# Kernel tuning notes

Hardware: AMD Instinct MI355X
Metric: run time of the kernel (lower is better)

Reference implementation:

```python
import jax, jax.numpy as jnp
import numpy as np
from jax import lax

V, E, H, L = 32000, 512, 512, 2
B, S, T = 64, 128, 64


def setup_inputs() -> dict:
    key = jax.random.key(0)
    ks = jax.random.split(key, 16)
    sc = 0.05  # weight scale to keep gates/tanh in a sane range
    inp = {
        "tokens": jax.random.randint(ks[0], (T, B), 0, V, dtype=jnp.int32),
        "memory_bank": jax.random.normal(ks[1], (B, S, H), dtype=jnp.float32),
        "lengths": jax.random.randint(ks[2], (B,), 1, S + 1, dtype=jnp.int32),
        "h0": jax.random.normal(ks[3], (L, B, H), dtype=jnp.float32),
        "c0": jax.random.normal(ks[4], (L, B, H), dtype=jnp.float32),
        "embedding": jax.random.normal(ks[5], (V, E), dtype=jnp.float32),
        "w_ih0": jax.random.normal(ks[6], (4 * H, E + H), dtype=jnp.float32) * sc,
        "w_hh0": jax.random.normal(ks[7], (4 * H, H), dtype=jnp.float32) * sc,
        "b_ih0": jax.random.normal(ks[8], (4 * H,), dtype=jnp.float32) * sc,
        "b_hh0": jax.random.normal(ks[9], (4 * H,), dtype=jnp.float32) * sc,
        "w_ih1": jax.random.normal(ks[10], (4 * H, H), dtype=jnp.float32) * sc,
        "w_hh1": jax.random.normal(ks[11], (4 * H, H), dtype=jnp.float32) * sc,
        "b_ih1": jax.random.normal(ks[12], (4 * H,), dtype=jnp.float32) * sc,
        "b_hh1": jax.random.normal(ks[13], (4 * H,), dtype=jnp.float32) * sc,
        "w_in": jax.random.normal(ks[14], (H, H), dtype=jnp.float32) * sc,
        "w_out": jax.random.normal(ks[15], (H, 2 * H), dtype=jnp.float32) * sc,
    }
    return inp


def _lstm_cell(x, h, c, w_ih, w_hh, b_ih, b_hh):
    # PyTorch LSTMCell: gates in (i, f, g, o) order
    g = x @ w_ih.T + b_ih + h @ w_hh.T + b_hh
    i, f, gg, o = jnp.split(g, 4, axis=-1)
    c_new = jax.nn.sigmoid(f) * c + jax.nn.sigmoid(i) * jnp.tanh(gg)
    h_new = jax.nn.sigmoid(o) * jnp.tanh(c_new)
    return h_new, c_new


def reference(tokens, memory_bank, lengths, h0, c0, embedding,
              w_ih0, w_hh0, b_ih0, b_hh0, w_ih1, w_hh1, b_ih1, b_hh1,
              w_in, w_out):
    Bn, Sn, Hn = memory_bank.shape
    mask = jnp.arange(Sn)[None, :] < lengths[:, None]  # [B, S]

    def step(carry, tok):
        h, c, feed = carry  # h, c: [L, B, H]; feed: [B, H]
        emb = jnp.take(embedding, tok, axis=0)           # [B, E]
        x = jnp.concatenate([emb, feed], axis=-1)        # [B, E+H]
        h0n, c0n = _lstm_cell(x, h[0], c[0], w_ih0, w_hh0, b_ih0, b_hh0)
        h1n, c1n = _lstm_cell(h0n, h[1], c[1], w_ih1, w_hh1, b_ih1, b_hh1)
        rnn_out = h1n                                    # [B, H]
        # Luong general attention
        q = rnn_out @ w_in.T                             # [B, H]
        scores = jnp.einsum('bh,bsh->bs', q, memory_bank)
        scores = jnp.where(mask, scores, -jnp.inf)
        p = jax.nn.softmax(scores, axis=-1)              # [B, S]
        ctx = jnp.einsum('bs,bsh->bh', p, memory_bank)   # [B, H]
        attn_h = jnp.tanh(jnp.concatenate([ctx, rnn_out], axis=-1) @ w_out.T)
        new_carry = (jnp.stack([h0n, h1n]), jnp.stack([c0n, c1n]), attn_h)
        return new_carry, (attn_h, p)

    feed0 = jnp.zeros((Bn, Hn), dtype=memory_bank.dtype)
    (h_f, c_f, _), (dec_outs, attns) = lax.scan(step, (h0, c0, feed0), tokens)
    return dec_outs, attns, h_f, c_f
```

## Files before the change

kernel.cpp:

```cpp
#include <hip/hip_runtime.h>
#include <hip/hip_bf16.h>

typedef __bf16 bf16x8 __attribute__((ext_vector_type(8)));
typedef unsigned short u16x8 __attribute__((ext_vector_type(8)));
typedef float f32x4 __attribute__((ext_vector_type(4)));

constexpr int TT = 64;
constexpr int BB = 64;
constexpr int SS = 128;
constexpr int HH = 512;
constexpr int GG = 2048;

constexpr int NW0E = 2048 * 512;
constexpr int NW0R = 2048 * 1024;
constexpr int NW1  = 2048 * 512;
constexpr int NWO  = 512 * 1024;
constexpr int NWI  = 512 * 512;

struct P {
  const int* tok; const float* mbank; const int* len;
  const float* h0_in; const float* c0_in; const float* emb;
  const float* w_ih0; const float* w_hh0; const float* b_ih0; const float* b_hh0;
  const float* w_ih1; const float* w_hh1; const float* b_ih1; const float* b_hh1;
  const float* w_in; const float* w_out;
  float* out_dec; float* out_attn; float* out_hf; float* out_cf;
  unsigned short *W0E, *W0R, *Wih1, *Whh1, *Wout, *WinT;
  float *EGb;
  float *Mw;
  float *b0, *b1, *h0buf, *h1s, *c0s, *c1s, *feed, *part1, *ctx, *scg;
  unsigned int* flag;
};

__device__ __forceinline__ unsigned short f2bf(float f) {
  unsigned int u = __builtin_bit_cast(unsigned int, f);
  return (unsigned short)((u + 0x7fffu + ((u >> 16) & 1u)) >> 16);
}
__device__ __forceinline__ float bf2f(unsigned short h) {
  return __builtin_bit_cast(float, ((unsigned int)h) << 16);
}
__device__ __forceinline__ bf16x8 ldb(const unsigned short* p) {
  return __builtin_bit_cast(bf16x8, *(const u16x8*)p);
}
__device__ __forceinline__ f32x4 mfma_(bf16x8 a, bf16x8 b, f32x4 c) {
  return __builtin_amdgcn_mfma_f32_16x16x32_bf16(a, b, c, 0, 0, 0);
}
__device__ __forceinline__ float sigm(float x) { return 1.f / (1.f + __expf(-x)); }
__device__ __forceinline__ f32x4 zero4() { f32x4 z = {0.f, 0.f, 0.f, 0.f}; return z; }

#define ATL(pp) __hip_atomic_load((pp), __ATOMIC_RELAXED, __HIP_MEMORY_SCOPE_AGENT)
#define ATS(pp, vv) __hip_atomic_store((pp), (vv), __ATOMIC_RELAXED, __HIP_MEMORY_SCOPE_AGENT)
#define ATA(pp, vv) __hip_atomic_fetch_add((pp), (vv), __ATOMIC_RELAXED, __HIP_MEMORY_SCOPE_AGENT)

__device__ __forceinline__ void splitA(const float* s, bf16x8& hi, bf16x8& lo) {
  float4 a0 = *(const float4*)s;
  float4 a1 = *(const float4*)(s + 4);
  float v[8] = {a0.x, a0.y, a0.z, a0.w, a1.x, a1.y, a1.z, a1.w};
  u16x8 h, l;
#pragma unroll
  for (int j = 0; j < 8; ++j) {
    unsigned short hb = f2bf(v[j]);
    h[j] = hb;
    l[j] = f2bf(v[j] - bf2f(hb));
  }
  hi = __builtin_bit_cast(bf16x8, h);
  lo = __builtin_bit_cast(bf16x8, l);
}
__device__ __forceinline__ f32x4 mfma3(bf16x8 ah, bf16x8 al, bf16x8 bh, bf16x8 bl, f32x4 c) {
  c = mfma_(al, bh, c);
  c = mfma_(ah, bl, c);
  c = mfma_(ah, bh, c);
  return c;
}

__global__ void prep_weights(P p) {
  constexpr int TOT = NW0E + NW0R + NW1 + NW1 + NWO + NWI + 2048 + 2048 +
                      32768 * 5 + 8192 + 1024;
  for (int i = blockIdx.x * blockDim.x + threadIdx.x; i < TOT;
       i += gridDim.x * blockDim.x) {
    int j = i;
    float v; unsigned short* dst; int N;
    if (j < NW0E) {
      int n = j >> 9, k = j & 511;
      v = p.w_ih0[n * 1024 + k];
      dst = p.W0E; N = NW0E; goto split;
    }
    j -= NW0E;
    if (j < NW0R) {
      int n = j >> 10, k = j & 1023;
      v = (k < 512) ? p.w_ih0[n * 1024 + 512 + k] : p.w_hh0[n * 512 + (k - 512)];
      dst = p.W0R; N = NW0R; goto split;
    }
    j -= NW0R;
    if (j < NW1) { v = p.w_ih1[j]; dst = p.Wih1; N = NW1; goto split; }
    j -= NW1;
    if (j < NW1) { v = p.w_hh1[j]; dst = p.Whh1; N = NW1; goto split; }
    j -= NW1;
    if (j < NWO) { v = p.w_out[j]; dst = p.Wout; N = NWO; goto split; }
    j -= NWO;
    if (j < NWI) {
      int n = j >> 9, q = j & 511;
      v = p.w_in[q * 512 + n];
      dst = p.WinT; N = NWI; goto split;
    }
    j -= NWI;
    if (j < 2048) { p.b0[j] = p.b_ih0[j] + p.b_hh0[j]; continue; }
    j -= 2048;
    if (j < 2048) { p.b1[j] = p.b_ih1[j] + p.b_hh1[j]; continue; }
    j -= 2048;
    if (j < 32768) { p.h0buf[j] = p.h0_in[j]; continue; }
    j -= 32768;
    if (j < 32768) { p.h1s[j] = p.h0_in[32768 + j]; continue; }
    j -= 32768;
    if (j < 32768) { p.c0s[j] = p.c0_in[j]; continue; }
    j -= 32768;
    if (j < 32768) { p.c1s[j] = p.c0_in[32768 + j]; continue; }
    j -= 32768;
    if (j < 32768) { p.feed[j] = 0.f; continue; }
    j -= 32768;
    if (j < 8192) { p.scg[j] = 0.f; continue; }
    j -= 8192;
    p.flag[j] = 0u;
    continue;
  split:
    {
      unsigned short hb = f2bf(v);
      dst[j] = hb;
      dst[N + j] = f2bf(v - bf2f(hb));
    }
  }
}

__global__ void prep_mw(P p) {
  const int wg = blockIdx.x;
  const int bm = wg & 127, bn = wg >> 7;
  const int tid = threadIdx.x, wave = tid >> 6, lane = tid & 63;
  const int arow = lane & 15, kq = (lane >> 4) * 8;
  const int m0 = bm * 64 + wave * 16;
  const int n0 = bn * 16;
  const float* A = p.mbank + (size_t)(m0 + arow) * HH;
  const unsigned short* Bp = p.WinT + (size_t)(n0 + arow) * HH + kq;
  f32x4 acc = zero4();
  for (int kk = 0; kk < HH; kk += 32) {
    bf16x8 ah, al;
    splitA(A + kk + kq, ah, al);
    acc = mfma3(ah, al, ldb(Bp + kk), ldb(Bp + NWI + kk), acc);
  }
  const int r0 = m0 + (lane >> 4) * 4;
#pragma unroll
  for (int r = 0; r < 4; ++r)
    p.Mw[(size_t)(r0 + r) * HH + n0 + arow] = acc[r];
}

__global__ void prep_eg(P p) {
  const int wg = blockIdx.x;
  const int bn = wg & 127, bm = wg >> 7;
  const int tid = threadIdx.x, wave = tid >> 6, lane = tid & 63;
  const int arow = lane & 15, kq = (lane >> 4) * 8;
  const int m0 = bm * 64 + wave * 16;
  const int n0 = bn * 16;
  const int token = p.tok[m0 + arow];
  const float* A = p.emb + (size_t)token * 512;
  const unsigned short* Bp = p.W0E + (size_t)(n0 + arow) * 512 + kq;
  f32x4 acc = zero4();
  for (int kk = 0; kk < 512; kk += 32) {
    bf16x8 ah, al;
    splitA(A + kk + kq, ah, al);
    acc = mfma3(ah, al, ldb(Bp + kk), ldb(Bp + NW0E + kk), acc);
  }
  const int r0 = m0 + (lane >> 4) * 4;
  const float bb = p.b0[n0 + arow];
#pragma unroll
  for (int r = 0; r < 4; ++r)
    p.EGb[(size_t)(r0 + r) * 2048 + n0 + arow] = acc[r] + bb;
}

__global__ void __launch_bounds__(256) decoder_main(P p) {
  const int wg = blockIdx.x, tid = threadIdx.x;
  const int wave = tid >> 6, lane = tid & 63;
  const int arow = lane & 15;
  const int kq = (lane >> 4) * 8;
  const int g = wg >> 6;
  const int u = wg & 63;
  unsigned nb = 0;

  __shared__ unsigned short MbHi[32][512];
  __shared__ unsigned short MbLo[32][512];
  __shared__ float Aslab[16][516];
  __shared__ float exch[4][16][16];
  __shared__ float scl[128];
  __shared__ float pl[128];

  const int attb = (g << 4) + (u >> 2);
  const int attq = u & 3;

  for (int idx = tid; idx < 32 * 512; idx += 256) {
    int r = idx >> 9, c = idx & 511;
    float v = p.mbank[(size_t)(attb * 128 + attq * 32 + r) * 512 + c];
    unsigned short hb = f2bf(v);
    MbHi[r][c] = hb;
    MbLo[r][c] = f2bf(v - bf2f(hb));
  }
  float mwreg[8][8];
  {
    const float* mwb = p.Mw + (size_t)(attb * 128 + attq * 32 + wave * 8) * 512 + lane * 8;
#pragma unroll
    for (int i = 0; i < 8; ++i) {
      float4 a = *(const float4*)(mwb + i * 512);
      float4 b = *(const float4*)(mwb + i * 512 + 4);
      mwreg[i][0] = a.x; mwreg[i][1] = a.y; mwreg[i][2] = a.z; mwreg[i][3] = a.w;
      mwreg[i][4] = b.x; mwreg[i][5] = b.y; mwreg[i][6] = b.z; mwreg[i][7] = b.w;
    }
  }

  const int w2 = (u < 32) ? u : u - 32;
  const int strip = w2;
  const int gate = wave;
  const int colj = strip * 16 + arow;
  const int rowbase = g * 16 * 512;

  unsigned* slots = p.flag + 128 + g * 128;
  auto gbar = [&]() {
    ++nb;
    asm volatile("s_waitcnt vmcnt(0)" ::: "memory");
    __syncthreads();
    if (tid == 0) ATS(&slots[u], nb);
    for (;;) {
      unsigned v = (tid < 64) ? ATL(&slots[tid]) : nb;
      if (__syncthreads_count((int)(v < nb)) == 0) break;
    }
  };

  auto stageC = [&](const float* base) {
    __syncthreads();
    float4 v[8];
    const float* ap[8];
#pragma unroll
    for (int j = 0; j < 8; ++j) {
      int idx = tid * 4 + j * 1024;
      ap[j] = base + (idx >> 9) * 512 + (idx & 511);
    }
#pragma unroll
    for (int j = 0; j < 8; ++j)
      asm volatile("global_load_dwordx4 %0, %1, off sc1" : "=v"(v[j]) : "v"(ap[j]));
    asm volatile("s_waitcnt vmcnt(0)" ::: "memory");
    __builtin_amdgcn_sched_barrier(0);
#pragma unroll
    for (int j = 0; j < 8; ++j) {
      int idx = tid * 4 + j * 1024;
      *(float4*)&Aslab[idx >> 9][idx & 511] = v[j];
    }
    __syncthreads();
  };
  auto gemm_half = [&](const unsigned short* whi, const unsigned short* wlo,
                       f32x4 acc) {
#pragma unroll 4
    for (int kk = 0; kk < 512; kk += 32) {
      bf16x8 ah, al;
      splitA(&Aslab[arow][kk + kq], ah, al);
      acc = mfma3(ah, al, ldb(whi + kk), ldb(wlo + kk), acc);
    }
    return acc;
  };

  for (int t = 0; t < TT; ++t) {
    const float* h0c = p.h0buf + (t & 1) * (BB * HH);
    float* h0n = p.h0buf + ((t + 1) & 1) * (BB * HH);

    if (u < 32) {
      const size_t wr = (size_t)(gate * 512 + colj) * 1024;
      f32x4 acc = zero4();
      stageC(p.feed + rowbase);
      acc = gemm_half(p.W0R + wr + kq, p.W0R + NW0R + wr + kq, acc);
      stageC(h0c + rowbase);
      acc = gemm_half(p.W0R + wr + 512 + kq, p.W0R + NW0R + wr + 512 + kq, acc);
      const float* eg =
          p.EGb + ((size_t)(t * 64 + g * 16)) * 2048 + gate * 512 + colj;
#pragma unroll
      for (int r = 0; r < 4; ++r) {
        acc[r] += eg[((lane >> 4) * 4 + r) * 2048];
        exch[gate][(lane >> 4) * 4 + r][arow] = acc[r];
      }
      __syncthreads();
      {
        int br = tid >> 4, nc = tid & 15;
        int idx = rowbase + br * 512 + strip * 16 + nc;
        float iv = sigm(exch[0][br][nc]);
        float fv = sigm(exch[1][br][nc]);
        float gv = tanhf(exch[2][br][nc]);
        float ov = sigm(exch[3][br][nc]);
        float cn = fv * p.c0s[idx] + iv * gv;
        p.c0s[idx] = cn;
        float hv = ov * tanhf(cn);
        ATS(&h0n[idx], hv);
        if (t == TT - 1) { p.out_cf[idx] = cn; p.out_hf[idx] = hv; }
      }
    } else {
      const size_t wr = (size_t)(gate * 512 + colj) * 512;
      stageC(p.h1s + rowbase);
      f32x4 acc = gemm_half(p.Whh1 + wr + kq, p.Whh1 + NW1 + wr + kq, zero4());
      const float bb = p.b1[gate * 512 + colj];
#pragma unroll
      for (int r = 0; r < 4; ++r)
        ATS(&p.part1[(g * 16 + (lane >> 4) * 4 + r) * 2048 + gate * 512 + colj],
            acc[r] + bb);
    }
    gbar();

    if (u < 32) {
      const size_t wr = (size_t)(gate * 512 + colj) * 512;
      stageC(h0n + rowbase);
      f32x4 acc = gemm_half(p.Wih1 + wr + kq, p.Wih1 + NW1 + wr + kq, zero4());
#pragma unroll
      for (int r = 0; r < 4; ++r) {
        acc[r] += ATL(&p.part1[(g * 16 + (lane >> 4) * 4 + r) * 2048 +
                               gate * 512 + colj]);
        exch[gate][(lane >> 4) * 4 + r][arow] = acc[r];
      }
      __syncthreads();
      {
        int br = tid >> 4, nc = tid & 15;
        int idx = rowbase + br * 512 + strip * 16 + nc;
        float iv = sigm(exch[0][br][nc]);
        float fv = sigm(exch[1][br][nc]);
        float gv = tanhf(exch[2][br][nc]);
        float ov = sigm(exch[3][br][nc]);
        float cn = fv * p.c1s[idx] + iv * gv;
        p.c1s[idx] = cn;
        float hv = ov * tanhf(cn);
        ATS(&p.h1s[idx], hv);
        if (t == TT - 1) { p.out_cf[BB * HH + idx] = cn; p.out_hf[BB * HH + idx] = hv; }
      }
    } else {
      int base = g * 8192 + (u - 32) * 256 + tid;
      ATS(&p.ctx[base], 0.f);
    }
    gbar();

    {
      float h8[8];
      {
        const float* hp = p.h1s + attb * 512 + lane * 8;
        float4 a, c;
        asm volatile("global_load_dwordx4 %0, %1, off sc1" : "=v"(a) : "v"(hp));
        asm volatile("global_load_dwordx4 %0, %1, off sc1" : "=v"(c) : "v"(hp + 4));
        asm volatile("s_waitcnt vmcnt(0)" ::: "memory");
        __builtin_amdgcn_sched_barrier(0);
        h8[0] = a.x; h8[1] = a.y; h8[2] = a.z; h8[3] = a.w;
        h8[4] = c.x; h8[5] = c.y; h8[6] = c.z; h8[7] = c.w;
      }
#pragma unroll
      for (int i = 0; i < 8; ++i) {
        const int sl = wave * 8 + i;
        float d = h8[0] * mwreg[i][0] + h8[1] * mwreg[i][1] +
                  h8[2] * mwreg[i][2] + h8[3] * mwreg[i][3] +
                  h8[4] * mwreg[i][4] + h8[5] * mwreg[i][5] +
                  h8[6] * mwreg[i][6] + h8[7] * mwreg[i][7];
#pragma unroll
        for (int o = 32; o; o >>= 1) d += __shfl_xor(d, o);
        if (lane == 0) ATS(&p.scg[attb * 128 + attq * 32 + sl], d);
      }
      asm volatile("s_waitcnt vmcnt(0)" ::: "memory");
      __syncthreads();
      if (tid == 0) {
        ATA(&p.flag[attb], 1u);
        const unsigned tgt = 4u * (unsigned)(t + 1);
        while (ATL(&p.flag[attb]) < tgt) __builtin_amdgcn_s_sleep(1);
      }
      __syncthreads();
      if (tid < 128) scl[tid] = ATL(&p.scg[attb * 128 + tid]);
      __syncthreads();
      if (wave == 0) {
        const int lenb = p.len[attb];
        float s0 = (lane < lenb) ? scl[lane] : -__builtin_inff();
        float s1 = (lane + 64 < lenb) ? scl[lane + 64] : -__builtin_inff();
        float mx = fmaxf(s0, s1);
#pragma unroll
        for (int o = 32; o; o >>= 1) mx = fmaxf(mx, __shfl_xor(mx, o));
        float e0 = (lane < lenb) ? __expf(s0 - mx) : 0.f;
        float e1 = (lane + 64 < lenb) ? __expf(s1 - mx) : 0.f;
        float sm = e0 + e1;
#pragma unroll
        for (int o = 32; o; o >>= 1) sm += __shfl_xor(sm, o);
        float inv = 1.f / sm;
        pl[lane] = e0 * inv; pl[lane + 64] = e1 * inv;
        if (attq == 0) {
          float* ao = p.out_attn + ((size_t)t * BB + attb) * SS;
          ao[lane] = e0 * inv; ao[lane + 64] = e1 * inv;
        }
      }
      __syncthreads();
      {
        const int h2 = tid * 2;
        float ca = 0.f, cb = 0.f;
#pragma unroll 4
        for (int s = 0; s < 32; ++s) {
          float ps = pl[attq * 32 + s];
          unsigned vh = *(const unsigned*)&MbHi[s][h2];
          unsigned vl = *(const unsigned*)&MbLo[s][h2];
          ca += ps * (bf2f((unsigned short)(vh & 0xffffu)) +
                      bf2f((unsigned short)(vl & 0xffffu)));
          cb += ps * (bf2f((unsigned short)(vh >> 16)) +
                      bf2f((unsigned short)(vl >> 16)));
        }
        atomicAdd(&p.ctx[attb * 512 + h2], ca);
        atomicAdd(&p.ctx[attb * 512 + h2 + 1], cb);
      }
    }
    gbar();

    if (u < 8) {
      const int nstrip = u * 4 + wave;
      const int cj = nstrip * 16 + arow;
      const size_t wr = (size_t)cj * 1024;
      f32x4 acc = zero4();
      stageC(p.ctx + rowbase);
      acc = gemm_half(p.Wout + wr + kq, p.Wout + NWO + wr + kq, acc);
      stageC(p.h1s + rowbase);
      acc = gemm_half(p.Wout + wr + 512 + kq, p.Wout + NWO + wr + 512 + kq, acc);
      float* dec = p.out_dec + (size_t)t * BB * HH;
#pragma unroll
      for (int r = 0; r < 4; ++r) {
        int b = g * 16 + (lane >> 4) * 4 + r;
        float v = tanhf(acc[r]);
        dec[b * 512 + cj] = v;
        ATS(&p.feed[b * 512 + cj], v);
      }
    }
    gbar();
  }
}

extern "C" void kernel_launch(void* const* d_in, const int* in_sizes, int n_in,
                              void* d_out, int out_size, void* d_ws, size_t ws_size,
                              hipStream_t stream) {
  P p;
  p.tok   = (const int*)d_in[0];
  p.mbank = (const float*)d_in[1];
  p.len   = (const int*)d_in[2];
  p.h0_in = (const float*)d_in[3];
  p.c0_in = (const float*)d_in[4];
  p.emb   = (const float*)d_in[5];
  p.w_ih0 = (const float*)d_in[6];
  p.w_hh0 = (const float*)d_in[7];
  p.b_ih0 = (const float*)d_in[8];
  p.b_hh0 = (const float*)d_in[9];
  p.w_ih1 = (const float*)d_in[10];
  p.w_hh1 = (const float*)d_in[11];
  p.b_ih1 = (const float*)d_in[12];
  p.b_hh1 = (const float*)d_in[13];
  p.w_in  = (const float*)d_in[14];
  p.w_out = (const float*)d_in[15];

  float* out = (float*)d_out;
  p.out_dec  = out;
  p.out_attn = out + (size_t)TT * BB * HH;
  p.out_hf   = out + (size_t)TT * BB * HH + (size_t)TT * BB * SS;
  p.out_cf   = p.out_hf + 2 * BB * HH;

  char* w = (char*)d_ws;
  auto alloc = [&](size_t n) { char* r = w; w += (n + 255) & ~(size_t)255; return r; };
  p.W0E   = (unsigned short*)alloc((size_t)NW0E * 2 * 2);
  p.W0R   = (unsigned short*)alloc((size_t)NW0R * 2 * 2);
  p.Wih1  = (unsigned short*)alloc((size_t)NW1 * 2 * 2);
  p.Whh1  = (unsigned short*)alloc((size_t)NW1 * 2 * 2);
  p.Wout  = (unsigned short*)alloc((size_t)NWO * 2 * 2);
  p.WinT  = (unsigned short*)alloc((size_t)NWI * 2 * 2);
  p.EGb   = (float*)alloc((size_t)4096 * 2048 * 4);
  p.Mw    = (float*)alloc((size_t)BB * SS * HH * 4);
  p.b0    = (float*)alloc(2048 * 4);
  p.b1    = (float*)alloc(2048 * 4);
  p.h0buf = (float*)alloc((size_t)2 * BB * HH * 4);
  p.h1s   = (float*)alloc((size_t)BB * HH * 4);
  p.c0s   = (float*)alloc((size_t)BB * HH * 4);
  p.c1s   = (float*)alloc((size_t)BB * HH * 4);
  p.feed  = (float*)alloc((size_t)BB * HH * 4);
  p.part1 = (float*)alloc((size_t)BB * GG * 4);
  p.ctx   = (float*)alloc((size_t)BB * HH * 4);
  p.scg   = (float*)alloc((size_t)BB * SS * 4);
  p.flag  = (unsigned int*)alloc(1024 * 4);

  hipLaunchKernelGGL(prep_weights, dim3(4096), dim3(256), 0, stream, p);
  hipLaunchKernelGGL(prep_mw, dim3(4096), dim3(256), 0, stream, p);
  hipLaunchKernelGGL(prep_eg, dim3(8192), dim3(256), 0, stream, p);

  void* args[] = {(void*)&p};
  hipError_t ce = hipLaunchCooperativeKernel((void*)decoder_main, dim3(256),
                                             dim3(256), args, 0, stream);
  if (ce != hipSuccess) {
    (void)hipGetLastError();
    hipLaunchKernelGGL(decoder_main, dim3(256), dim3(256), 0, stream, p);
  }
}
```

Measured before the change: 3.525 ms.

## Fuse output projection into attention blocks with per-batch flag sync

```diff
diff --git a/kernel.cpp b/kernel.cpp
--- a/kernel.cpp
+++ b/kernel.cpp
@@ -24,7 +24,8 @@
   const float* w_ih1; const float* w_hh1; const float* b_ih1; const float* b_hh1;
   const float* w_in; const float* w_out;
   float* out_dec; float* out_attn; float* out_hf; float* out_cf;
-  unsigned short *W0E, *W0R, *Wih1, *Whh1, *Wout, *WinT;
+  unsigned short *W0E, *W0R, *Wih1, *Whh1, *WinT;
+  float *WoutT;
   float *EGb;
   float *Mw;
   float *b0, *b1, *h0buf, *h1s, *c0s, *c1s, *feed, *part1, *ctx, *scg;
@@ -95,7 +96,11 @@
     j -= NW1;
     if (j < NW1) { v = p.w_hh1[j]; dst = p.Whh1; N = NW1; goto split; }
     j -= NW1;
-    if (j < NWO) { v = p.w_out[j]; dst = p.Wout; N = NWO; goto split; }
+    if (j < NWO) {
+      int k = j >> 9, n = j & 511;
+      p.WoutT[j] = p.w_out[n * 1024 + k];
+      continue;
+    }
     j -= NWO;
     if (j < NWI) {
       int n = j >> 9, q = j & 511;
@@ -189,6 +194,7 @@
   __shared__ float exch[4][16][16];
   __shared__ float scl[128];
   __shared__ float pl[128];
+  __shared__ float prj[1024];
 
   const int attb = (g << 4) + (u >> 2);
   const int attq = u & 3;
@@ -229,6 +235,15 @@
       if (__syncthreads_count((int)(v < nb)) == 0) break;
     }
   };
+  auto fsync = [&](unsigned* f, unsigned tgt) {
+    asm volatile("s_waitcnt vmcnt(0)" ::: "memory");
+    __syncthreads();
+    if (tid == 0) {
+      ATA(f, 1u);
+      while (ATL(f) < tgt) __builtin_amdgcn_s_sleep(1);
+    }
+    __syncthreads();
+  };
 
   auto stageC = [&](const float* base) {
     __syncthreads();
@@ -268,16 +283,19 @@
 
     if (u < 32) {
       const size_t wr = (size_t)(gate * 512 + colj) * 1024;
+      const float* eg =
+          p.EGb + ((size_t)(t * 64 + g * 16)) * 2048 + gate * 512 + colj;
+      float egv[4];
+#pragma unroll
+      for (int r = 0; r < 4; ++r) egv[r] = eg[((lane >> 4) * 4 + r) * 2048];
       f32x4 acc = zero4();
       stageC(p.feed + rowbase);
       acc = gemm_half(p.W0R + wr + kq, p.W0R + NW0R + wr + kq, acc);
       stageC(h0c + rowbase);
       acc = gemm_half(p.W0R + wr + 512 + kq, p.W0R + NW0R + wr + 512 + kq, acc);
-      const float* eg =
-          p.EGb + ((size_t)(t * 64 + g * 16)) * 2048 + gate * 512 + colj;
 #pragma unroll
       for (int r = 0; r < 4; ++r) {
-        acc[r] += eg[((lane >> 4) * 4 + r) * 2048];
+        acc[r] += egv[r];
         exch[gate][(lane >> 4) * 4 + r][arow] = acc[r];
       }
       __syncthreads();
@@ -308,12 +326,16 @@
 
     if (u < 32) {
       const size_t wr = (size_t)(gate * 512 + colj) * 512;
+      float pv[4];
+#pragma unroll
+      for (int r = 0; r < 4; ++r)
+        pv[r] = ATL(&p.part1[(g * 16 + (lane >> 4) * 4 + r) * 2048 +
+                             gate * 512 + colj]);
       stageC(h0n + rowbase);
       f32x4 acc = gemm_half(p.Wih1 + wr + kq, p.Wih1 + NW1 + wr + kq, zero4());
 #pragma unroll
       for (int r = 0; r < 4; ++r) {
-        acc[r] += ATL(&p.part1[(g * 16 + (lane >> 4) * 4 + r) * 2048 +
-                               gate * 512 + colj]);
+        acc[r] += pv[r];
         exch[gate][(lane >> 4) * 4 + r][arow] = acc[r];
       }
       __syncthreads();
@@ -359,14 +381,7 @@
         for (int o = 32; o; o >>= 1) d += __shfl_xor(d, o);
         if (lane == 0) ATS(&p.scg[attb * 128 + attq * 32 + sl], d);
       }
-      asm volatile("s_waitcnt vmcnt(0)" ::: "memory");
-      __syncthreads();
-      if (tid == 0) {
-        ATA(&p.flag[attb], 1u);
-        const unsigned tgt = 4u * (unsigned)(t + 1);
-        while (ATL(&p.flag[attb]) < tgt) __builtin_amdgcn_s_sleep(1);
-      }
-      __syncthreads();
+      fsync(&p.flag[attb], 4u * (unsigned)(t + 1));
       if (tid < 128) scl[tid] = ATL(&p.scg[attb * 128 + tid]);
       __syncthreads();
       if (wave == 0) {
@@ -387,6 +402,8 @@
           float* ao = p.out_attn + ((size_t)t * BB + attb) * SS;
           ao[lane] = e0 * inv; ao[lane + 64] = e1 * inv;
         }
+        *(float4*)&prj[512 + lane * 8]     = make_float4(h8[0], h8[1], h8[2], h8[3]);
+        *(float4*)&prj[512 + lane * 8 + 4] = make_float4(h8[4], h8[5], h8[6], h8[7]);
       }
       __syncthreads();
       {
@@ -405,25 +422,29 @@
         atomicAdd(&p.ctx[attb * 512 + h2], ca);
         atomicAdd(&p.ctx[attb * 512 + h2 + 1], cb);
       }
-    }
-    gbar();
-
-    if (u < 8) {
-      const int nstrip = u * 4 + wave;
-      const int cj = nstrip * 16 + arow;
-      const size_t wr = (size_t)cj * 1024;
-      f32x4 acc = zero4();
-      stageC(p.ctx + rowbase);
-      acc = gemm_half(p.Wout + wr + kq, p.Wout + NWO + wr + kq, acc);
-      stageC(p.h1s + rowbase);
-      acc = gemm_half(p.Wout + wr + 512 + kq, p.Wout + NWO + wr + 512 + kq, acc);
-      float* dec = p.out_dec + (size_t)t * BB * HH;
-#pragma unroll
-      for (int r = 0; r < 4; ++r) {
-        int b = g * 16 + (lane >> 4) * 4 + r;
-        float v = tanhf(acc[r]);
-        dec[b * 512 + cj] = v;
-        ATS(&p.feed[b * 512 + cj], v);
+      fsync(&p.flag[64 + attb], 4u * (unsigned)(t + 1));
+      {
+        prj[tid * 2]     = ATL(&p.ctx[attb * 512 + tid * 2]);
+        prj[tid * 2 + 1] = ATL(&p.ctx[attb * 512 + tid * 2 + 1]);
+      }
+      __syncthreads();
+      {
+        const int jc = attq * 128 + (tid & 127);
+        const int kh = tid >> 7;
+        const float* wt = p.WoutT + jc;
+        float d = 0.f;
+#pragma unroll 8
+        for (int k = kh * 512; k < kh * 512 + 512; ++k)
+          d = fmaf(prj[k], wt[(size_t)k * 512], d);
+        float* exf = (float*)exch;
+        if (kh == 1) exf[tid - 128] = d;
+        __syncthreads();
+        if (kh == 0) {
+          d += exf[tid];
+          float v = tanhf(d);
+          p.out_dec[(size_t)t * BB * HH + attb * 512 + jc] = v;
+          ATS(&p.feed[attb * 512 + jc], v);
+        }
       }
     }
     gbar();
@@ -463,8 +484,8 @@
   p.W0R   = (unsigned short*)alloc((size_t)NW0R * 2 * 2);
   p.Wih1  = (unsigned short*)alloc((size_t)NW1 * 2 * 2);
   p.Whh1  = (unsigned short*)alloc((size_t)NW1 * 2 * 2);
-  p.Wout  = (unsigned short*)alloc((size_t)NWO * 2 * 2);
   p.WinT  = (unsigned short*)alloc((size_t)NWI * 2 * 2);
+  p.WoutT = (float*)alloc((size_t)NWO * 4);
   p.EGb   = (float*)alloc((size_t)4096 * 2048 * 4);
   p.Mw    = (float*)alloc((size_t)BB * SS * HH * 4);
   p.b0    = (float*)alloc(2048 * 4);
```

Measured after the change: 3.563 ms. About the same (+1.1%).
